# Optimization experiments

Hardware: AMD Instinct MI355X
Metric: run time of the kernel (lower is better)

## Reference

```python
import jax, jax.numpy as jnp
import numpy as np
from jax import lax

B, L = 8, 1024
C_IN, D_MODEL = 3, 512
N_MAMBA, N_TRANS, NHEAD = 2, 2, 8
D_STATE, D_CONV, EXPAND = 16, 4, 2
DI = EXPAND * D_MODEL            # 1024, mamba inner dim
DT_RANK = D_MODEL // 16          # 32
DH = D_MODEL // NHEAD            # 64, head dim
DFF = 4 * D_MODEL


def setup_inputs() -> dict:
    key = jax.random.key(0)
    ks = iter(jax.random.split(key, 64))
    def rn(shape, s=0.05):
        return jax.random.normal(next(ks), shape, jnp.float32) * s
    inp = {
        'x': jax.random.normal(next(ks), (B, C_IN, L), jnp.float32),
        'proj_w': rn((D_MODEL, C_IN)), 'proj_b': rn((D_MODEL,)),
        # stacked per-mamba-layer params (leading dim = N_MAMBA)
        'm_in_w': rn((N_MAMBA, 2 * DI, D_MODEL)),
        'm_conv_w': rn((N_MAMBA, DI, D_CONV)), 'm_conv_b': rn((N_MAMBA, DI)),
        'm_xproj_w': rn((N_MAMBA, DT_RANK + 2 * D_STATE, DI)),
        'm_dt_w': rn((N_MAMBA, DI, DT_RANK)), 'm_dt_b': rn((N_MAMBA, DI)),
        'm_Alog': jnp.tile(jnp.log(jnp.arange(1, D_STATE + 1, dtype=jnp.float32)), (N_MAMBA, DI, 1)),
        'm_D': jnp.ones((N_MAMBA, DI), jnp.float32),
        'm_out_w': rn((N_MAMBA, D_MODEL, DI)),
        'm_ln_w': jnp.ones((N_MAMBA, D_MODEL), jnp.float32), 'm_ln_b': jnp.zeros((N_MAMBA, D_MODEL), jnp.float32),
        # stacked per-transformer-layer params
        't_qkv_w': rn((N_TRANS, 3 * D_MODEL, D_MODEL)), 't_qkv_b': rn((N_TRANS, 3 * D_MODEL)),
        't_ow': rn((N_TRANS, D_MODEL, D_MODEL)), 't_ob': rn((N_TRANS, D_MODEL)),
        't_l1w': rn((N_TRANS, DFF, D_MODEL)), 't_l1b': rn((N_TRANS, DFF)),
        't_l2w': rn((N_TRANS, D_MODEL, DFF)), 't_l2b': rn((N_TRANS, D_MODEL)),
        't_ln1w': jnp.ones((N_TRANS, D_MODEL), jnp.float32), 't_ln1b': jnp.zeros((N_TRANS, D_MODEL), jnp.float32),
        't_ln2w': jnp.ones((N_TRANS, D_MODEL), jnp.float32), 't_ln2b': jnp.zeros((N_TRANS, D_MODEL), jnp.float32),
        'no_w': jnp.ones((D_MODEL,), jnp.float32), 'no_b': jnp.zeros((D_MODEL,), jnp.float32),
    }
    return inp


def _ln(x, w, b, eps=1e-5):
    m = x.mean(-1, keepdims=True)
    v = ((x - m) ** 2).mean(-1, keepdims=True)
    return (x - m) / jnp.sqrt(v + eps) * w + b


def _pos_encoding(length, d):
    pos = jnp.arange(length, dtype=jnp.float32)[:, None]
    div = jnp.exp(jnp.arange(0, d, 2, dtype=jnp.float32) * (-np.log(10000.0) / d))
    pe = jnp.zeros((length, d), jnp.float32)
    pe = pe.at[:, 0::2].set(jnp.sin(pos * div)).at[:, 1::2].set(jnp.cos(pos * div))
    return pe


def _mamba(h, in_w, conv_w, conv_b, xp_w, dt_w, dt_b, Alog, Dp, out_w):
    # h: [B,L,d_model]
    xz = h @ in_w.T                                   # [B,L,2*DI]
    xm, z = jnp.split(xz, 2, axis=-1)
    # causal depthwise conv1d over time
    k = conv_w.T[:, None, :]                          # [D_CONV,1,DI]
    xc = lax.conv_general_dilated(xm, k, (1,), [(D_CONV - 1, 0)],
                                  dimension_numbers=('NWC', 'WIO', 'NWC'),
                                  feature_group_count=DI) + conv_b
    xc = jax.nn.silu(xc)
    xdb = xc @ xp_w.T                                 # [B,L,DT_RANK+2*D_STATE]
    dt = jax.nn.softplus(xdb[..., :DT_RANK] @ dt_w.T + dt_b)   # [B,L,DI]
    Bm = xdb[..., DT_RANK:DT_RANK + D_STATE]          # [B,L,D_STATE]
    Cm = xdb[..., DT_RANK + D_STATE:]                 # [B,L,D_STATE]
    A = -jnp.exp(Alog)                                # [DI,D_STATE]

    def step(state, t):
        dt_t, B_t, C_t, x_t = t                       # [B,DI],[B,S],[B,S],[B,DI]
        dA = jnp.exp(dt_t[..., None] * A)             # [B,DI,S]
        state = state * dA + (dt_t * x_t)[..., None] * B_t[:, None, :]
        y = jnp.einsum('bds,bs->bd', state, C_t)
        return state, y

    init = jnp.zeros((h.shape[0], DI, D_STATE), h.dtype)
    seq = (dt.transpose(1, 0, 2), Bm.transpose(1, 0, 2), Cm.transpose(1, 0, 2), xc.transpose(1, 0, 2))
    _, ys = lax.scan(step, init, seq)                 # ys: [L,B,DI]
    y = ys.transpose(1, 0, 2) + Dp * xc
    y = y * jax.nn.silu(z)
    return y @ out_w.T                                # [B,L,d_model]


def _transformer_layer(h, qkv_w, qkv_b, ow, ob, l1w, l1b, l2w, l2b, ln1w, ln1b, ln2w, ln2b):
    Bt, Lt, d = h.shape
    qkv = h @ qkv_w.T + qkv_b
    q, k, v = jnp.split(qkv, 3, axis=-1)
    q = q.reshape(Bt, Lt, NHEAD, DH); k = k.reshape(Bt, Lt, NHEAD, DH); v = v.reshape(Bt, Lt, NHEAD, DH)
    sc = jnp.einsum('blhd,bmhd->bhlm', q, k) / np.sqrt(DH).astype(np.float32)
    a = jax.nn.softmax(sc, axis=-1)
    o = jnp.einsum('bhlm,bmhd->blhd', a, v).reshape(Bt, Lt, d)
    h = _ln(h + o @ ow.T + ob, ln1w, ln1b)
    ff = jax.nn.relu(h @ l1w.T + l1b) @ l2w.T + l2b
    return _ln(h + ff, ln2w, ln2b)


def reference(x, proj_w, proj_b, m_in_w, m_conv_w, m_conv_b, m_xproj_w, m_dt_w, m_dt_b,
              m_Alog, m_D, m_out_w, m_ln_w, m_ln_b, t_qkv_w, t_qkv_b, t_ow, t_ob,
              t_l1w, t_l1b, t_l2w, t_l2b, t_ln1w, t_ln1b, t_ln2w, t_ln2b, no_w, no_b):
    # proj_in: 1x1 conv == pointwise linear over channels; output [B,L,d]
    h = jnp.einsum('bcl,dc->bld', x, proj_w) + proj_b
    for i in range(N_MAMBA):
        h = _ln(h + _mamba(h, m_in_w[i], m_conv_w[i], m_conv_b[i], m_xproj_w[i],
                           m_dt_w[i], m_dt_b[i], m_Alog[i], m_D[i], m_out_w[i]),
                m_ln_w[i], m_ln_b[i])
    h = h + _pos_encoding(h.shape[1], D_MODEL)
    for i in range(N_TRANS):
        h = _transformer_layer(h, t_qkv_w[i], t_qkv_b[i], t_ow[i], t_ob[i],
                               t_l1w[i], t_l1b[i], t_l2w[i], t_l2b[i],
                               t_ln1w[i], t_ln1b[i], t_ln2w[i], t_ln2b[i])
    h = _ln(h, no_w, no_b)
    return h, h.mean(axis=1)
```

## Files before the change

### kernel.cpp

```cpp
#include <hip/hip_runtime.h>
#include <cstddef>

#define BATCH 8
#define LSEQ 1024
#define DMODEL 512
#define DINNER 1024
#define DSTATE 16
#define DTRANK 32
#define NHEAD 8
#define DHEAD 64
#define DFF 2048
#define MTOK 8192
#define NCHUNK 16
#define CLEN 64

typedef __attribute__((ext_vector_type(8))) short bfrag;
typedef __attribute__((ext_vector_type(4))) float f32x4;
typedef __attribute__((ext_vector_type(4))) unsigned short us4;
typedef unsigned short ushort_t;

__device__ __forceinline__ float silu_f(float x) { return x / (1.f + __expf(-x)); }

__device__ __forceinline__ unsigned short f2bf(float f) {
  unsigned u = __float_as_uint(f);
  return (unsigned short)((u + 0x7FFFu + ((u >> 16) & 1u)) >> 16);
}
__device__ __forceinline__ float bf2f(ushort_t u) {
  return __uint_as_float((unsigned)u << 16);
}

__device__ __forceinline__ void gll16(const ushort_t* g, ushort_t* l) {
  __builtin_amdgcn_global_load_lds(
      (const __attribute__((address_space(1))) unsigned int*)g,
      (__attribute__((address_space(3))) unsigned int*)l, 16, 0, 0);
}

__global__ __launch_bounds__(256) void cvt_bf16(const float* __restrict__ s,
                                                ushort_t* __restrict__ d, int n4) {
  int i = blockIdx.x * 256 + threadIdx.x;
  if (i >= n4) return;
  float4 v = ((const float4*)s)[i];
  us4 o = {f2bf(v.x), f2bf(v.y), f2bf(v.z), f2bf(v.w)};
  ((us4*)d)[i] = o;
}

__global__ __launch_bounds__(256) void proj_kernel(const float* __restrict__ x,
                                                   const float* __restrict__ pw,
                                                   const float* __restrict__ pb,
                                                   float* __restrict__ h,
                                                   ushort_t* __restrict__ hbf) {
  int idx = blockIdx.x * 256 + threadIdx.x;
  int d = idx & 511;
  int l = (idx >> 9) & 1023;
  int b = idx >> 19;
  const float* xb = x + (size_t)b * 3 * 1024 + l;
  float v = pb[d] + xb[0] * pw[d * 3] + xb[1024] * pw[d * 3 + 1] + xb[2048] * pw[d * 3 + 2];
  h[idx] = v;
  hbf[idx] = f2bf(v);
}

template <int ACT, int CBF, int SPLITK, int BN>
__global__ __launch_bounds__(256) void gemm_gll(const ushort_t* __restrict__ A,
                                                const ushort_t* __restrict__ W,
                                                const float* __restrict__ bias,
                                                void* __restrict__ Cp,
                                                int K, int lda, int ldc) {
  __shared__ ushort_t sA[2][4096];
  __shared__ ushort_t sB[2][BN * 32];
  constexpr int MREP = (BN == 128) ? 4 : 2;
  const int bm = blockIdx.y * 128, bn = blockIdx.x * BN;
  const int tid = threadIdx.x;
  const int wid = tid >> 6, lane = tid & 63;
  const int wrb = (BN == 128) ? (wid >> 1) * 64 : wid * 32;
  const int wcb = (BN == 128) ? (wid & 1) * 64 : 0;
  const int lr = lane & 15, ls = lane >> 4;
  const int sw = ls ^ ((lr >> 1) & 3);

  const int kseg = K / SPLITK;
  const int kbeg = (SPLITK > 1) ? blockIdx.z * kseg : 0;

  const int c0 = wid * 128 + lane;
  const int c1 = c0 + 64;
  const int r0 = c0 >> 2, s0 = (c0 & 3) ^ ((r0 >> 1) & 3);
  const int r1 = c1 >> 2, s1 = (c1 & 3) ^ ((r1 >> 1) & 3);
  const ushort_t* gA0 = A + (size_t)(bm + r0) * lda + kbeg + s0 * 8;
  const ushort_t* gA1 = A + (size_t)(bm + r1) * lda + kbeg + s1 * 8;
  const ushort_t* gB0;
  const ushort_t* gB1 = nullptr;
  if constexpr (BN == 128) {
    gB0 = W + (size_t)(bn + r0) * K + kbeg + s0 * 8;
    gB1 = W + (size_t)(bn + r1) * K + kbeg + s1 * 8;
  } else {
    const int cb = wid * 64 + lane;
    const int rb = cb >> 2, sb2 = (cb & 3) ^ ((rb >> 1) & 3);
    gB0 = W + (size_t)(bn + rb) * K + kbeg + sb2 * 8;
  }

  f32x4 acc[MREP][4];
#pragma unroll
  for (int i = 0; i < MREP; ++i)
#pragma unroll
    for (int j = 0; j < 4; ++j) acc[i][j] = (f32x4)(0.f);

#define STAGE(buf, step)                                             \
  do {                                                               \
    gll16(gA0 + (step) * 32, &sA[buf][wid * 1024]);                  \
    gll16(gA1 + (step) * 32, &sA[buf][wid * 1024 + 512]);            \
    if constexpr (BN == 128) {                                       \
      gll16(gB0 + (step) * 32, &sB[buf][wid * 1024]);                \
      gll16(gB1 + (step) * 32, &sB[buf][wid * 1024 + 512]);          \
    } else {                                                         \
      gll16(gB0 + (step) * 32, &sB[buf][wid * 512]);                 \
    }                                                                \
  } while (0)

  const int NT = kseg / 32;
  STAGE(0, 0);
  for (int t = 0; t < NT; ++t) {
    const int cur = t & 1;
    if (t + 1 < NT) {
      STAGE(cur ^ 1, t + 1);
      if constexpr (BN == 128)
        asm volatile("s_waitcnt vmcnt(4)" ::: "memory");
      else
        asm volatile("s_waitcnt vmcnt(3)" ::: "memory");
    } else {
      asm volatile("s_waitcnt vmcnt(0)" ::: "memory");
    }
    __builtin_amdgcn_sched_barrier(0);
    __builtin_amdgcn_s_barrier();
    __builtin_amdgcn_sched_barrier(0);

    bfrag af[MREP], bf[4];
#pragma unroll
    for (int mi = 0; mi < MREP; ++mi) {
      int row = wrb + mi * 16 + lr;
      af[mi] = *(const bfrag*)&sA[cur][(size_t)((row << 2) + sw) * 8];
    }
#pragma unroll
    for (int nj = 0; nj < 4; ++nj) {
      int col = wcb + nj * 16 + lr;
      bf[nj] = *(const bfrag*)&sB[cur][(size_t)((col << 2) + sw) * 8];
    }
#pragma unroll
    for (int mi = 0; mi < MREP; ++mi)
#pragma unroll
      for (int nj = 0; nj < 4; ++nj)
        acc[mi][nj] = __builtin_amdgcn_mfma_f32_16x16x32_bf16(af[mi], bf[nj], acc[mi][nj], 0, 0, 0);

    __builtin_amdgcn_s_barrier();
    __builtin_amdgcn_sched_barrier(0);
  }
#undef STAGE

  if (SPLITK > 1) {
    float* Cz = (float*)Cp + (size_t)blockIdx.z * 8192 * ldc;
#pragma unroll
    for (int nj = 0; nj < 4; ++nj) {
      int col = bn + wcb + nj * 16 + lr;
#pragma unroll
      for (int mi = 0; mi < MREP; ++mi) {
        int row0 = bm + wrb + mi * 16 + ls * 4;
#pragma unroll
        for (int r = 0; r < 4; ++r)
          Cz[(size_t)(row0 + r) * ldc + col] = acc[mi][nj][r];
      }
    }
  } else {
#pragma unroll
    for (int nj = 0; nj < 4; ++nj) {
      int col = bn + wcb + nj * 16 + lr;
      float bv = bias ? bias[col] : 0.f;
#pragma unroll
      for (int mi = 0; mi < MREP; ++mi) {
        int row0 = bm + wrb + mi * 16 + ls * 4;
#pragma unroll
        for (int r = 0; r < 4; ++r) {
          float v = acc[mi][nj][r] + bv;
          if (ACT == 1) v = fmaxf(v, 0.f);
          if (ACT == 2) v = (v > 20.f) ? v : log1pf(__expf(v));
          if (CBF)
            ((ushort_t*)Cp)[(size_t)(row0 + r) * ldc + col] = f2bf(v);
          else
            ((float*)Cp)[(size_t)(row0 + r) * ldc + col] = v;
        }
      }
    }
  }
}

__global__ __launch_bounds__(256) void reduce8_xdb(const float* __restrict__ p,
                                                   float* __restrict__ xdb,
                                                   ushort_t* __restrict__ xdb_bf) {
  int i = blockIdx.x * 256 + threadIdx.x;
  float4 a = ((const float4*)p)[i];
#pragma unroll
  for (int z = 1; z < 8; ++z) {
    float4 b = ((const float4*)p)[i + z * 131072];
    a.x += b.x; a.y += b.y; a.z += b.z; a.w += b.w;
  }
  ((float4*)xdb)[i] = a;
  us4 o = {f2bf(a.x), f2bf(a.y), f2bf(a.z), f2bf(a.w)};
  ((us4*)xdb_bf)[i] = o;
}

__global__ __launch_bounds__(256) void conv_silu_kernel(const ushort_t* __restrict__ xz,
                                                        const float* __restrict__ cw,
                                                        const float* __restrict__ cb,
                                                        ushort_t* __restrict__ xc) {
  int idx = blockIdx.x * 256 + threadIdx.x;
  int d = idx & 1023;
  int t = (idx >> 10) & 1023;
  int b = idx >> 20;
  float acc = cb[d];
#pragma unroll
  for (int w = 0; w < 4; ++w) {
    int tt = t - 3 + w;
    if (tt >= 0) acc += bf2f(xz[(((size_t)(b * 1024 + tt)) << 11) + d]) * cw[d * 4 + w];
  }
  xc[idx] = f2bf(silu_f(acc));
}

__global__ __launch_bounds__(256) void scan_pass1(const float* __restrict__ dt,
                                                  const float* __restrict__ xdb,
                                                  const ushort_t* __restrict__ xc,
                                                  const float* __restrict__ Alog,
                                                  float* __restrict__ scrP,
                                                  float* __restrict__ scrL) {
  int idx = blockIdx.x * 256 + threadIdx.x;
  int sh = idx & 3;
  int d = (idx >> 2) & 1023;
  int c = (idx >> 12) & 15;
  int b = idx >> 16;
  float A[4], st[4], P[4];
#pragma unroll
  for (int s = 0; s < 4; ++s) {
    A[s] = -__expf(Alog[d * 16 + sh * 4 + s]);
    st[s] = 0.f;
    P[s] = 1.f;
  }
  int t0 = c * CLEN;
  size_t base = (((size_t)(b * 1024 + t0)) << 10) + d;
  const float* xb = xdb + (size_t)(b * 1024 + t0) * 64 + 32 + sh * 4;
  float dtv = dt[base], xv = bf2f(xc[base]);
  for (int t = 0; t < CLEN; ++t) {
    float dtn = 0.f, xvn = 0.f;
    if (t + 1 < CLEN) { dtn = dt[base + 1024]; xvn = bf2f(xc[base + 1024]); }
    float4 Bv = *(const float4*)xb;
    float dx = dtv * xv;
    float e0 = __expf(dtv * A[0]), e1 = __expf(dtv * A[1]);
    float e2 = __expf(dtv * A[2]), e3 = __expf(dtv * A[3]);
    st[0] = st[0] * e0 + dx * Bv.x; P[0] *= e0;
    st[1] = st[1] * e1 + dx * Bv.y; P[1] *= e1;
    st[2] = st[2] * e2 + dx * Bv.z; P[2] *= e2;
    st[3] = st[3] * e3 + dx * Bv.w; P[3] *= e3;
    base += 1024; xb += 64;
    dtv = dtn; xv = xvn;
  }
  size_t pbase = (((size_t)((b * 16 + c) * 16 + sh * 4)) << 10) + d;
#pragma unroll
  for (int s = 0; s < 4; ++s) {
    scrP[pbase + ((size_t)s << 10)] = P[s];
    scrL[pbase + ((size_t)s << 10)] = st[s];
  }
}

__global__ __launch_bounds__(256) void scan_pass2(const float* __restrict__ scrP,
                                                  float* __restrict__ scrL) {
  int idx = blockIdx.x * 256 + threadIdx.x;
  int d = idx & 1023;
  int s = (idx >> 10) & 15;
  int b = idx >> 14;
  float cur = 0.f;
  for (int c = 0; c < 16; ++c) {
    size_t o = (((size_t)(((b * 16 + c) * 16) + s)) << 10) + d;
    float P = scrP[o];
    float loc = scrL[o];
    scrL[o] = cur;
    cur = cur * P + loc;
  }
}

__global__ __launch_bounds__(256) void scan_pass3(const float* __restrict__ dt,
                                                  const float* __restrict__ xdb,
                                                  const ushort_t* __restrict__ xc,
                                                  const ushort_t* __restrict__ xz,
                                                  ushort_t* __restrict__ ybf,
                                                  const float* __restrict__ Alog,
                                                  const float* __restrict__ Dp,
                                                  const float* __restrict__ scrL) {
  int idx = blockIdx.x * 256 + threadIdx.x;
  int sh = idx & 3;
  int d = (idx >> 2) & 1023;
  int c = (idx >> 12) & 15;
  int b = idx >> 16;
  float A[4], st[4];
  size_t pbase = (((size_t)((b * 16 + c) * 16 + sh * 4)) << 10) + d;
#pragma unroll
  for (int s = 0; s < 4; ++s) {
    A[s] = -__expf(Alog[d * 16 + sh * 4 + s]);
    st[s] = scrL[pbase + ((size_t)s << 10)];
  }
  float Dv = Dp[d];
  int t0 = c * CLEN;
  size_t base = (((size_t)(b * 1024 + t0)) << 10) + d;
  size_t zoff = ((((size_t)(b * 1024 + t0)) << 11)) + 1024 + d;
  const float* xb = xdb + (size_t)(b * 1024 + t0) * 64 + 32 + sh * 4;
  float dtv = dt[base], xv = bf2f(xc[base]), zv = bf2f(xz[zoff]);
  for (int t = 0; t < CLEN; ++t) {
    float dtn = 0.f, xvn = 0.f, zvn = 0.f;
    if (t + 1 < CLEN) {
      dtn = dt[base + 1024]; xvn = bf2f(xc[base + 1024]); zvn = bf2f(xz[zoff + 2048]);
    }
    float4 Bv = *(const float4*)xb;
    float4 Cv = *(const float4*)(xb + 16);
    float dx = dtv * xv;
    float e0 = __expf(dtv * A[0]), e1 = __expf(dtv * A[1]);
    float e2 = __expf(dtv * A[2]), e3 = __expf(dtv * A[3]);
    st[0] = st[0] * e0 + dx * Bv.x;
    st[1] = st[1] * e1 + dx * Bv.y;
    st[2] = st[2] * e2 + dx * Bv.z;
    st[3] = st[3] * e3 + dx * Bv.w;
    float acc = st[0] * Cv.x + st[1] * Cv.y + st[2] * Cv.z + st[3] * Cv.w;
    acc += __shfl_xor(acc, 1);
    acc += __shfl_xor(acc, 2);
    if (sh == 0)
      ybf[base] = f2bf((acc + Dv * xv) * silu_f(zv));
    base += 1024; zoff += 2048; xb += 64;
    dtv = dtn; xv = xvn; zv = zvn;
  }
}

__global__ __launch_bounds__(128) void resid_ln_kernel(const float* __restrict__ x,
                                                       const float* __restrict__ add,
                                                       const float* __restrict__ w,
                                                       const float* __restrict__ bias,
                                                       float* __restrict__ out,
                                                       ushort_t* __restrict__ out_bf) {
  int row = blockIdx.x, tid = threadIdx.x;
  float4 v = ((const float4*)(x + (size_t)row * 512))[tid];
  if (add) {
    float4 a = ((const float4*)(add + (size_t)row * 512))[tid];
    v.x += a.x; v.y += a.y; v.z += a.z; v.w += a.w;
  }
  float s = v.x + v.y + v.z + v.w;
  float ss = v.x * v.x + v.y * v.y + v.z * v.z + v.w * v.w;
#pragma unroll
  for (int o = 32; o; o >>= 1) {
    s += __shfl_xor(s, o);
    ss += __shfl_xor(ss, o);
  }
  __shared__ float red[4];
  int wid = tid >> 6;
  if ((tid & 63) == 0) { red[wid] = s; red[2 + wid] = ss; }
  __syncthreads();
  s = red[0] + red[1];
  ss = red[2] + red[3];
  float mean = s * (1.f / 512.f);
  float var = ss * (1.f / 512.f) - mean * mean;
  float inv = rsqrtf(var + 1e-5f);
  float4 wv = ((const float4*)w)[tid];
  float4 bv = ((const float4*)bias)[tid];
  float4 ov;
  ov.x = (v.x - mean) * inv * wv.x + bv.x;
  ov.y = (v.y - mean) * inv * wv.y + bv.y;
  ov.z = (v.z - mean) * inv * wv.z + bv.z;
  ov.w = (v.w - mean) * inv * wv.w + bv.w;
  ((float4*)(out + (size_t)row * 512))[tid] = ov;
  if (out_bf) {
    us4 ob = {f2bf(ov.x), f2bf(ov.y), f2bf(ov.z), f2bf(ov.w)};
    ((us4*)(out_bf + (size_t)row * 512))[tid] = ob;
  }
}

__global__ __launch_bounds__(128) void resid_ln_sk(const float* __restrict__ x,
                                                   const float* __restrict__ p,
                                                   const float* __restrict__ pbias,
                                                   const float* __restrict__ w,
                                                   const float* __restrict__ bias,
                                                   float* __restrict__ out,
                                                   ushort_t* __restrict__ out_bf) {
  int row = blockIdx.x, tid = threadIdx.x;
  float4 v = ((const float4*)(x + (size_t)row * 512))[tid];
  float4 a = ((const float4*)(p + (size_t)row * 512))[tid];
  float4 c = ((const float4*)(p + 4194304 + (size_t)row * 512))[tid];
  v.x += a.x + c.x; v.y += a.y + c.y; v.z += a.z + c.z; v.w += a.w + c.w;
  if (pbias) {
    float4 pb = ((const float4*)pbias)[tid];
    v.x += pb.x; v.y += pb.y; v.z += pb.z; v.w += pb.w;
  }
  float s = v.x + v.y + v.z + v.w;
  float ss = v.x * v.x + v.y * v.y + v.z * v.z + v.w * v.w;
#pragma unroll
  for (int o = 32; o; o >>= 1) {
    s += __shfl_xor(s, o);
    ss += __shfl_xor(ss, o);
  }
  __shared__ float red[4];
  int wid = tid >> 6;
  if ((tid & 63) == 0) { red[wid] = s; red[2 + wid] = ss; }
  __syncthreads();
  s = red[0] + red[1];
  ss = red[2] + red[3];
  float mean = s * (1.f / 512.f);
  float var = ss * (1.f / 512.f) - mean * mean;
  float inv = rsqrtf(var + 1e-5f);
  float4 wv = ((const float4*)w)[tid];
  float4 bv = ((const float4*)bias)[tid];
  float4 ov;
  ov.x = (v.x - mean) * inv * wv.x + bv.x;
  ov.y = (v.y - mean) * inv * wv.y + bv.y;
  ov.z = (v.z - mean) * inv * wv.z + bv.z;
  ov.w = (v.w - mean) * inv * wv.w + bv.w;
  ((float4*)(out + (size_t)row * 512))[tid] = ov;
  us4 ob = {f2bf(ov.x), f2bf(ov.y), f2bf(ov.z), f2bf(ov.w)};
  ((us4*)(out_bf + (size_t)row * 512))[tid] = ob;
}

__global__ __launch_bounds__(256) void posenc_kernel(float* __restrict__ h,
                                                     ushort_t* __restrict__ hbf) {
  int idx = blockIdx.x * 256 + threadIdx.x;
  int d = idx & 511;
  int l = (idx >> 9) & 1023;
  float freq = __expf(-(float)(d & ~1) * (9.210340371976184f / 512.f));
  float ang = (float)l * freq;
  float v = h[idx] + ((d & 1) ? cosf(ang) : sinf(ang));
  h[idx] = v;
  hbf[idx] = f2bf(v);
}

__global__ __launch_bounds__(256) void attn_mfma(const ushort_t* __restrict__ qkv,
                                                 ushort_t* __restrict__ ao) {
  __shared__ unsigned short Qs[8192];
  __shared__ unsigned short Ks[4096];
  __shared__ unsigned short Vt[4096];
  __shared__ unsigned short Ps[4096];
  const int tid = threadIdx.x;
  const int blk = blockIdx.x;
  const int qt = blk & 7, hh = (blk >> 3) & 7, b = blk >> 6;
  const int l0 = qt * 128;
  const size_t bb = (size_t)b * 1024 * 1536;

  const int srow = tid >> 2;
  const int sdb = (tid & 3) << 4;
  const int sc0 = sdb >> 3;

  {
    const ushort_t* qp = qkv + bb + (size_t)(l0 + srow) * 1536 + hh * 64 + sdb;
    *(bfrag*)&Qs[srow * 64 + ((sc0 ^ (srow & 7)) << 3)] = *(const bfrag*)qp;
    *(bfrag*)&Qs[srow * 64 + (((sc0 + 1) ^ (srow & 7)) << 3)] = *(const bfrag*)(qp + 8);
    const ushort_t* qp2 = qp + (size_t)64 * 1536;
    *(bfrag*)&Qs[(srow + 64) * 64 + ((sc0 ^ (srow & 7)) << 3)] = *(const bfrag*)qp2;
    *(bfrag*)&Qs[(srow + 64) * 64 + (((sc0 + 1) ^ (srow & 7)) << 3)] = *(const bfrag*)(qp2 + 8);
  }
  __syncthreads();

  const int wid = tid >> 6, lane = tid & 63;
  const int l15 = lane & 15, rg = lane >> 4;
  const int l7 = l15 & 7;

  bfrag aq[2][2];
#pragma unroll
  for (int s = 0; s < 2; ++s)
#pragma unroll
    for (int ks = 0; ks < 2; ++ks) {
      int qr = wid * 32 + s * 16 + l15;
      aq[s][ks] = *(const bfrag*)&Qs[qr * 64 + (((ks * 4 + rg) ^ l7) << 3)];
    }

  float m[2][4], lsum[2][4];
  f32x4 oacc[2][4];
#pragma unroll
  for (int s = 0; s < 2; ++s)
#pragma unroll
    for (int r = 0; r < 4; ++r) { m[s][r] = -1e30f; lsum[s][r] = 0.f; }
#pragma unroll
  for (int s = 0; s < 2; ++s)
#pragma unroll
    for (int nt = 0; nt < 4; ++nt) oacc[s][nt] = (f32x4)(0.f);

  for (int jt = 0; jt < 16; ++jt) {
    {
      const ushort_t* kp = qkv + bb + (size_t)(jt * 64 + srow) * 1536 + hh * 64 + 512 + sdb;
      *(bfrag*)&Ks[srow * 64 + ((sc0 ^ (srow & 7)) << 3)] = *(const bfrag*)kp;
      *(bfrag*)&Ks[srow * 64 + (((sc0 + 1) ^ (srow & 7)) << 3)] = *(const bfrag*)(kp + 8);
      const ushort_t* vp = kp + 512;
      unsigned short vv[16];
      *(bfrag*)&vv[0] = *(const bfrag*)vp;
      *(bfrag*)&vv[8] = *(const bfrag*)(vp + 8);
#pragma unroll
      for (int j = 0; j < 16; ++j) {
        int dd = sdb + j;
        Vt[dd * 64 + (((srow >> 3) ^ (dd & 7)) << 3) + (srow & 7)] = vv[j];
      }
    }
    __syncthreads();

#pragma unroll
    for (int s = 0; s < 2; ++s) {
      f32x4 sc[4];
#pragma unroll
      for (int nt = 0; nt < 4; ++nt) {
        f32x4 sv = (f32x4)(0.f);
#pragma unroll
        for (int ks = 0; ks < 2; ++ks) {
          bfrag bk = *(const bfrag*)&Ks[(nt * 16 + l15) * 64 + (((ks * 4 + rg) ^ l7) << 3)];
          sv = __builtin_amdgcn_mfma_f32_16x16x32_bf16(aq[s][ks], bk, sv, 0, 0, 0);
        }
        sc[nt] = sv * 0.125f;
      }

#pragma unroll
      for (int r = 0; r < 4; ++r) {
        float mc = fmaxf(fmaxf(sc[0][r], sc[1][r]), fmaxf(sc[2][r], sc[3][r]));
#pragma unroll
        for (int o = 8; o; o >>= 1) mc = fmaxf(mc, __shfl_xor(mc, o));
        float mn = fmaxf(m[s][r], mc);
        float al = __expf(m[s][r] - mn);
        m[s][r] = mn;
        int prow = rg * 4 + r;
        float ps = 0.f;
#pragma unroll
        for (int nt = 0; nt < 4; ++nt) {
          float p = __expf(sc[nt][r] - mn);
          ps += p;
          int col = nt * 16 + l15;
          Ps[wid * 1024 + prow * 64 + ((((col >> 3) ^ (prow & 7))) << 3) + (col & 7)] = f2bf(p);
        }
#pragma unroll
        for (int o = 8; o; o >>= 1) ps += __shfl_xor(ps, o);
        lsum[s][r] = lsum[s][r] * al + ps;
#pragma unroll
        for (int nt = 0; nt < 4; ++nt) oacc[s][nt][r] *= al;
      }

      bfrag ap[2];
#pragma unroll
      for (int ks = 0; ks < 2; ++ks)
        ap[ks] = *(const bfrag*)&Ps[wid * 1024 + l15 * 64 + (((ks * 4 + rg) ^ l7) << 3)];
#pragma unroll
      for (int nt = 0; nt < 4; ++nt) {
#pragma unroll
        for (int ks = 0; ks < 2; ++ks) {
          bfrag bv = *(const bfrag*)&Vt[(nt * 16 + l15) * 64 + (((ks * 4 + rg) ^ l7) << 3)];
          oacc[s][nt] = __builtin_amdgcn_mfma_f32_16x16x32_bf16(ap[ks], bv, oacc[s][nt], 0, 0, 0);
        }
      }
    }
    __syncthreads();
  }

#pragma unroll
  for (int s = 0; s < 2; ++s)
#pragma unroll
    for (int r = 0; r < 4; ++r) {
      float inv = 1.f / lsum[s][r];
      int row = l0 + wid * 32 + s * 16 + rg * 4 + r;
      ushort_t* op = ao + ((size_t)(b * 1024 + row)) * 512 + hh * 64;
#pragma unroll
      for (int nt = 0; nt < 4; ++nt) op[nt * 16 + l15] = f2bf(oacc[s][nt][r] * inv);
    }
}

__global__ __launch_bounds__(512) void mean_part(const float* __restrict__ h,
                                                 float* __restrict__ part) {
  int blk = blockIdx.x;
  int b = blk >> 4, lc = blk & 15, d = threadIdx.x;
  float s = 0.f;
  int l0 = lc * 64;
  for (int l = l0; l < l0 + 64; ++l) s += h[(((size_t)(b * 1024 + l)) << 9) + d];
  part[((size_t)blk << 9) + d] = s;
}
__global__ __launch_bounds__(256) void mean_final(const float* __restrict__ part,
                                                  float* __restrict__ out2) {
  int i = blockIdx.x * 256 + threadIdx.x;
  int b = i >> 9, d = i & 511;
  float s = 0.f;
#pragma unroll
  for (int c = 0; c < 16; ++c) s += part[(((size_t)(b * 16 + c)) << 9) + d];
  out2[i] = s * (1.f / 1024.f);
}

extern "C" void kernel_launch(void* const* d_in, const int* in_sizes, int n_in,
                              void* d_out, int out_size, void* d_ws, size_t ws_size,
                              hipStream_t stream) {
  const float* x        = (const float*)d_in[0];
  const float* proj_w   = (const float*)d_in[1];
  const float* proj_b   = (const float*)d_in[2];
  const float* m_in_w   = (const float*)d_in[3];
  const float* m_conv_w = (const float*)d_in[4];
  const float* m_conv_b = (const float*)d_in[5];
  const float* m_xproj_w= (const float*)d_in[6];
  const float* m_dt_w   = (const float*)d_in[7];
  const float* m_dt_b   = (const float*)d_in[8];
  const float* m_Alog   = (const float*)d_in[9];
  const float* m_D      = (const float*)d_in[10];
  const float* m_out_w  = (const float*)d_in[11];
  const float* m_ln_w   = (const float*)d_in[12];
  const float* m_ln_b   = (const float*)d_in[13];
  const float* t_qkv_w  = (const float*)d_in[14];
  const float* t_qkv_b  = (const float*)d_in[15];
  const float* t_ow     = (const float*)d_in[16];
  const float* t_ob     = (const float*)d_in[17];
  const float* t_l1w    = (const float*)d_in[18];
  const float* t_l1b    = (const float*)d_in[19];
  const float* t_l2w    = (const float*)d_in[20];
  const float* t_l2b    = (const float*)d_in[21];
  const float* t_ln1w   = (const float*)d_in[22];
  const float* t_ln1b   = (const float*)d_in[23];
  const float* t_ln2w   = (const float*)d_in[24];
  const float* t_ln2b   = (const float*)d_in[25];
  const float* no_w     = (const float*)d_in[26];
  const float* no_b     = (const float*)d_in[27];

  float* ws   = (float*)d_ws;
  float* h    = ws;
  ushort_t* h_bf = (ushort_t*)(ws + 4194304);
  float* bufA = ws + 6291456;
  float* bufB = bufA + 16777216;
  float* bufC = bufB + 8388608;
  float* bufE = bufC + 8388608;
  float* bufF = bufE + 4194304;
  ushort_t* y_bf = (ushort_t*)(bufF + 524288);
  ushort_t* wbf  = (ushort_t*)(bufF + 524288 + 4194304);
  float* scrP = bufE;
  float* scrL = bufE + 2097152;

  ushort_t* wIN  = wbf;
  ushort_t* wOUT = wbf + 2097152;
  ushort_t* wQKV = wbf + 3145728;
  ushort_t* wOW  = wbf + 4718592;
  ushort_t* wL1  = wbf + 5242880;
  ushort_t* wL2  = wbf + 7340032;
  ushort_t* wXP  = wbf + 9437184;
  ushort_t* wDT  = wbf + 9568256;
  ushort_t* xdb_bf = wbf + 9633792;

  cvt_bf16<<<2048, 256, 0, stream>>>(m_in_w,  wIN,  524288);
  cvt_bf16<<<1024, 256, 0, stream>>>(m_out_w, wOUT, 262144);
  cvt_bf16<<<1536, 256, 0, stream>>>(t_qkv_w, wQKV, 393216);
  cvt_bf16<<< 512, 256, 0, stream>>>(t_ow,    wOW,  131072);
  cvt_bf16<<<2048, 256, 0, stream>>>(t_l1w,   wL1,  524288);
  cvt_bf16<<<2048, 256, 0, stream>>>(t_l2w,   wL2,  524288);
  cvt_bf16<<< 128, 256, 0, stream>>>(m_xproj_w, wXP, 32768);
  cvt_bf16<<<  64, 256, 0, stream>>>(m_dt_w,  wDT,  16384);

  proj_kernel<<<16384, 256, 0, stream>>>(x, proj_w, proj_b, h, h_bf);

  for (int i = 0; i < 2; ++i) {
    gemm_gll<0, 1, 1, 128><<<dim3(16, 64), 256, 0, stream>>>(
        h_bf, wIN + (size_t)i * 1048576, nullptr, bufA, DMODEL, DMODEL, 2 * DINNER);
    conv_silu_kernel<<<32768, 256, 0, stream>>>((const ushort_t*)bufA,
                                                m_conv_w + i * DINNER * 4,
                                                m_conv_b + i * DINNER, (ushort_t*)bufB);
    gemm_gll<0, 0, 8, 64><<<dim3(1, 64, 8), 256, 0, stream>>>(
        (const ushort_t*)bufB, wXP + (size_t)i * 65536, nullptr, bufC,
        DINNER, DINNER, 64);
    reduce8_xdb<<<512, 256, 0, stream>>>(bufC, bufF, xdb_bf);
    gemm_gll<2, 0, 1, 128><<<dim3(8, 64), 256, 0, stream>>>(
        xdb_bf, wDT + (size_t)i * 32768, m_dt_b + i * DINNER, bufC,
        DTRANK, 64, DINNER);
    scan_pass1<<<2048, 256, 0, stream>>>(bufC, bufF, (const ushort_t*)bufB,
                                         m_Alog + (size_t)i * DINNER * DSTATE, scrP, scrL);
    scan_pass2<<<512, 256, 0, stream>>>(scrP, scrL);
    scan_pass3<<<2048, 256, 0, stream>>>(bufC, bufF, (const ushort_t*)bufB,
                                         (const ushort_t*)bufA, y_bf,
                                         m_Alog + (size_t)i * DINNER * DSTATE,
                                         m_D + i * DINNER, scrL);
    gemm_gll<0, 0, 2, 128><<<dim3(4, 64, 2), 256, 0, stream>>>(
        y_bf, wOUT + (size_t)i * 524288, nullptr, bufC, DINNER, DINNER, DMODEL);
    resid_ln_sk<<<8192, 128, 0, stream>>>(h, bufC, nullptr, m_ln_w + i * DMODEL,
                                          m_ln_b + i * DMODEL, h, h_bf);
  }

  posenc_kernel<<<16384, 256, 0, stream>>>(h, h_bf);

  for (int i = 0; i < 2; ++i) {
    gemm_gll<0, 1, 1, 128><<<dim3(12, 64), 256, 0, stream>>>(
        h_bf, wQKV + (size_t)i * 786432, t_qkv_b + i * 3 * DMODEL, bufA,
        DMODEL, DMODEL, 3 * DMODEL);
    attn_mfma<<<512, 256, 0, stream>>>((const ushort_t*)bufA, (ushort_t*)bufB);
    gemm_gll<0, 0, 2, 128><<<dim3(4, 64, 2), 256, 0, stream>>>(
        (const ushort_t*)bufB, wOW + (size_t)i * 262144, nullptr, bufC,
        DMODEL, DMODEL, DMODEL);
    resid_ln_sk<<<8192, 128, 0, stream>>>(h, bufC, t_ob + i * DMODEL,
                                          t_ln1w + i * DMODEL, t_ln1b + i * DMODEL, h, h_bf);
    gemm_gll<1, 1, 1, 128><<<dim3(16, 64), 256, 0, stream>>>(
        h_bf, wL1 + (size_t)i * 1048576, t_l1b + i * DFF, bufA,
        DMODEL, DMODEL, DFF);
    gemm_gll<0, 0, 2, 128><<<dim3(4, 64, 2), 256, 0, stream>>>(
        (const ushort_t*)bufA, wL2 + (size_t)i * 1048576, nullptr, bufC,
        DFF, DFF, DMODEL);
    resid_ln_sk<<<8192, 128, 0, stream>>>(h, bufC, t_l2b + i * DMODEL,
                                          t_ln2w + i * DMODEL, t_ln2b + i * DMODEL, h, h_bf);
  }

  float* out_h = (float*)d_out;
  resid_ln_kernel<<<8192, 128, 0, stream>>>(h, nullptr, no_w, no_b, out_h, nullptr);
  mean_part<<<128, 512, 0, stream>>>(out_h, bufF);
  mean_final<<<16, 256, 0, stream>>>(bufF, out_h + 4194304);
}
```

Baseline: 963.8 us.

## Batch weight conversions, store dt in bf16, shrink attention query tile

The eight weight-conversion launches become one segmented kernel that picks its source and destination by block index, which removes launch overhead. The dt projection GEMM now writes bf16 instead of fp32, and both scan passes read bf16 dt, which halves that traffic at some cost in precision. The attention kernel drops from 128 to 64 query rows per block and doubles the grid to 1024 blocks, with a block-to-(batch,head) mapping and an extra XOR swizzle on the V transpose to cut LDS bank conflicts. This trades more K/V reloads for more parallelism and lower register pressure.

```diff
diff --git a/kernel.cpp b/kernel.cpp
--- a/kernel.cpp
+++ b/kernel.cpp
@@ -35,13 +35,21 @@
       (__attribute__((address_space(3))) unsigned int*)l, 16, 0, 0);
 }
 
-__global__ __launch_bounds__(256) void cvt_bf16(const float* __restrict__ s,
-                                                ushort_t* __restrict__ d, int n4) {
-  int i = blockIdx.x * 256 + threadIdx.x;
-  if (i >= n4) return;
-  float4 v = ((const float4*)s)[i];
+struct Cvt8Args {
+  const float* s[8];
+  ushort_t* d[8];
+  int end[8];
+};
+__global__ __launch_bounds__(256) void cvt8(Cvt8Args a) {
+  int blk = blockIdx.x;
+  int seg = 0, start = 0;
+#pragma unroll
+  for (int i = 0; i < 7; ++i)
+    if (blk >= a.end[i]) { seg = i + 1; start = a.end[i]; }
+  int i4 = (blk - start) * 256 + threadIdx.x;
+  float4 v = ((const float4*)a.s[seg])[i4];
   us4 o = {f2bf(v.x), f2bf(v.y), f2bf(v.z), f2bf(v.w)};
-  ((us4*)d)[i] = o;
+  ((us4*)a.d[seg])[i4] = o;
 }
 
 __global__ __launch_bounds__(256) void proj_kernel(const float* __restrict__ x,
@@ -221,7 +229,7 @@
   xc[idx] = f2bf(silu_f(acc));
 }
 
-__global__ __launch_bounds__(256) void scan_pass1(const float* __restrict__ dt,
+__global__ __launch_bounds__(256) void scan_pass1(const ushort_t* __restrict__ dt,
                                                   const float* __restrict__ xdb,
                                                   const ushort_t* __restrict__ xc,
                                                   const float* __restrict__ Alog,
@@ -242,10 +250,10 @@
   int t0 = c * CLEN;
   size_t base = (((size_t)(b * 1024 + t0)) << 10) + d;
   const float* xb = xdb + (size_t)(b * 1024 + t0) * 64 + 32 + sh * 4;
-  float dtv = dt[base], xv = bf2f(xc[base]);
+  float dtv = bf2f(dt[base]), xv = bf2f(xc[base]);
   for (int t = 0; t < CLEN; ++t) {
     float dtn = 0.f, xvn = 0.f;
-    if (t + 1 < CLEN) { dtn = dt[base + 1024]; xvn = bf2f(xc[base + 1024]); }
+    if (t + 1 < CLEN) { dtn = bf2f(dt[base + 1024]); xvn = bf2f(xc[base + 1024]); }
     float4 Bv = *(const float4*)xb;
     float dx = dtv * xv;
     float e0 = __expf(dtv * A[0]), e1 = __expf(dtv * A[1]);
@@ -281,7 +289,7 @@
   }
 }
 
-__global__ __launch_bounds__(256) void scan_pass3(const float* __restrict__ dt,
+__global__ __launch_bounds__(256) void scan_pass3(const ushort_t* __restrict__ dt,
                                                   const float* __restrict__ xdb,
                                                   const ushort_t* __restrict__ xc,
                                                   const ushort_t* __restrict__ xz,
@@ -306,11 +314,11 @@
   size_t base = (((size_t)(b * 1024 + t0)) << 10) + d;
   size_t zoff = ((((size_t)(b * 1024 + t0)) << 11)) + 1024 + d;
   const float* xb = xdb + (size_t)(b * 1024 + t0) * 64 + 32 + sh * 4;
-  float dtv = dt[base], xv = bf2f(xc[base]), zv = bf2f(xz[zoff]);
+  float dtv = bf2f(dt[base]), xv = bf2f(xc[base]), zv = bf2f(xz[zoff]);
   for (int t = 0; t < CLEN; ++t) {
     float dtn = 0.f, xvn = 0.f, zvn = 0.f;
     if (t + 1 < CLEN) {
-      dtn = dt[base + 1024]; xvn = bf2f(xc[base + 1024]); zvn = bf2f(xz[zoff + 2048]);
+      dtn = bf2f(dt[base + 1024]); xvn = bf2f(xc[base + 1024]); zvn = bf2f(xz[zoff + 2048]);
     }
     float4 Bv = *(const float4*)xb;
     float4 Cv = *(const float4*)(xb + 16);
@@ -431,14 +439,16 @@
 
 __global__ __launch_bounds__(256) void attn_mfma(const ushort_t* __restrict__ qkv,
                                                  ushort_t* __restrict__ ao) {
-  __shared__ unsigned short Qs[8192];
+  __shared__ unsigned short Qs[4096];
   __shared__ unsigned short Ks[4096];
   __shared__ unsigned short Vt[4096];
   __shared__ unsigned short Ps[4096];
   const int tid = threadIdx.x;
-  const int blk = blockIdx.x;
-  const int qt = blk & 7, hh = (blk >> 3) & 7, b = blk >> 6;
-  const int l0 = qt * 128;
+  const int w = blockIdx.x;
+  const int bh = (w & 7) + (w >> 7) * 8;
+  const int qt = (w >> 3) & 15;
+  const int hh = bh & 7, b = bh >> 3;
+  const int l0 = qt * 64;
   const size_t bb = (size_t)b * 1024 * 1536;
 
   const int srow = tid >> 2;
@@ -449,35 +459,17 @@
     const ushort_t* qp = qkv + bb + (size_t)(l0 + srow) * 1536 + hh * 64 + sdb;
     *(bfrag*)&Qs[srow * 64 + ((sc0 ^ (srow & 7)) << 3)] = *(const bfrag*)qp;
     *(bfrag*)&Qs[srow * 64 + (((sc0 + 1) ^ (srow & 7)) << 3)] = *(const bfrag*)(qp + 8);
-    const ushort_t* qp2 = qp + (size_t)64 * 1536;
-    *(bfrag*)&Qs[(srow + 64) * 64 + ((sc0 ^ (srow & 7)) << 3)] = *(const bfrag*)qp2;
-    *(bfrag*)&Qs[(srow + 64) * 64 + (((sc0 + 1) ^ (srow & 7)) << 3)] = *(const bfrag*)(qp2 + 8);
-  }
-  __syncthreads();
+  }
 
   const int wid = tid >> 6, lane = tid & 63;
   const int l15 = lane & 15, rg = lane >> 4;
   const int l7 = l15 & 7;
-
-  bfrag aq[2][2];
-#pragma unroll
-  for (int s = 0; s < 2; ++s)
-#pragma unroll
-    for (int ks = 0; ks < 2; ++ks) {
-      int qr = wid * 32 + s * 16 + l15;
-      aq[s][ks] = *(const bfrag*)&Qs[qr * 64 + (((ks * 4 + rg) ^ l7) << 3)];
-    }
-
-  float m[2][4], lsum[2][4];
-  f32x4 oacc[2][4];
-#pragma unroll
-  for (int s = 0; s < 2; ++s)
-#pragma unroll
-    for (int r = 0; r < 4; ++r) { m[s][r] = -1e30f; lsum[s][r] = 0.f; }
-#pragma unroll
-  for (int s = 0; s < 2; ++s)
-#pragma unroll
-    for (int nt = 0; nt < 4; ++nt) oacc[s][nt] = (f32x4)(0.f);
+  float m[4], lsum[4];
+  f32x4 oacc[4];
+#pragma unroll
+  for (int r = 0; r < 4; ++r) { m[r] = -1e30f; lsum[r] = 0.f; }
+#pragma unroll
+  for (int nt = 0; nt < 4; ++nt) oacc[nt] = (f32x4)(0.f);
 
   for (int jt = 0; jt < 16; ++jt) {
     {
@@ -491,75 +483,76 @@
 #pragma unroll
       for (int j = 0; j < 16; ++j) {
         int dd = sdb + j;
-        Vt[dd * 64 + (((srow >> 3) ^ (dd & 7)) << 3) + (srow & 7)] = vv[j];
+        Vt[dd * 64 + (((srow >> 3) ^ (dd & 7) ^ ((dd >> 3) & 7)) << 3) + (srow & 7)] = vv[j];
       }
     }
     __syncthreads();
 
-#pragma unroll
-    for (int s = 0; s < 2; ++s) {
-      f32x4 sc[4];
+    bfrag aq[2];
+#pragma unroll
+    for (int ks = 0; ks < 2; ++ks)
+      aq[ks] = *(const bfrag*)&Qs[(wid * 16 + l15) * 64 + (((ks * 4 + rg) ^ l7) << 3)];
+    f32x4 sc[4];
+#pragma unroll
+    for (int nt = 0; nt < 4; ++nt) {
+      f32x4 s = (f32x4)(0.f);
+#pragma unroll
+      for (int ks = 0; ks < 2; ++ks) {
+        bfrag bk = *(const bfrag*)&Ks[(nt * 16 + l15) * 64 + (((ks * 4 + rg) ^ l7) << 3)];
+        s = __builtin_amdgcn_mfma_f32_16x16x32_bf16(aq[ks], bk, s, 0, 0, 0);
+      }
+      sc[nt] = s * 0.125f;
+    }
+
+#pragma unroll
+    for (int r = 0; r < 4; ++r) {
+      float mc = fmaxf(fmaxf(sc[0][r], sc[1][r]), fmaxf(sc[2][r], sc[3][r]));
+#pragma unroll
+      for (int o = 8; o; o >>= 1) mc = fmaxf(mc, __shfl_xor(mc, o));
+      float mn = fmaxf(m[r], mc);
+      float al = __expf(m[r] - mn);
+      m[r] = mn;
+      int prow = rg * 4 + r;
+      float ps = 0.f;
 #pragma unroll
       for (int nt = 0; nt < 4; ++nt) {
-        f32x4 sv = (f32x4)(0.f);
-#pragma unroll
-        for (int ks = 0; ks < 2; ++ks) {
-          bfrag bk = *(const bfrag*)&Ks[(nt * 16 + l15) * 64 + (((ks * 4 + rg) ^ l7) << 3)];
-          sv = __builtin_amdgcn_mfma_f32_16x16x32_bf16(aq[s][ks], bk, sv, 0, 0, 0);
-        }
-        sc[nt] = sv * 0.125f;
+        float p = __expf(sc[nt][r] - mn);
+        ps += p;
+        int col = nt * 16 + l15;
+        Ps[wid * 1024 + prow * 64 + ((((col >> 3) ^ (prow & 7))) << 3) + (col & 7)] = f2bf(p);
       }
-
-#pragma unroll
-      for (int r = 0; r < 4; ++r) {
-        float mc = fmaxf(fmaxf(sc[0][r], sc[1][r]), fmaxf(sc[2][r], sc[3][r]));
-#pragma unroll
-        for (int o = 8; o; o >>= 1) mc = fmaxf(mc, __shfl_xor(mc, o));
-        float mn = fmaxf(m[s][r], mc);
-        float al = __expf(m[s][r] - mn);
-        m[s][r] = mn;
-        int prow = rg * 4 + r;
-        float ps = 0.f;
-#pragma unroll
-        for (int nt = 0; nt < 4; ++nt) {
-          float p = __expf(sc[nt][r] - mn);
-          ps += p;
-          int col = nt * 16 + l15;
-          Ps[wid * 1024 + prow * 64 + ((((col >> 3) ^ (prow & 7))) << 3) + (col & 7)] = f2bf(p);
-        }
-#pragma unroll
-        for (int o = 8; o; o >>= 1) ps += __shfl_xor(ps, o);
-        lsum[s][r] = lsum[s][r] * al + ps;
-#pragma unroll
-        for (int nt = 0; nt < 4; ++nt) oacc[s][nt][r] *= al;
+#pragma unroll
+      for (int o = 8; o; o >>= 1) ps += __shfl_xor(ps, o);
+      lsum[r] = lsum[r] * al + ps;
+#pragma unroll
+      for (int nt = 0; nt < 4; ++nt) oacc[nt][r] *= al;
+    }
+
+    bfrag ap[2];
+#pragma unroll
+    for (int ks = 0; ks < 2; ++ks)
+      ap[ks] = *(const bfrag*)&Ps[wid * 1024 + l15 * 64 + (((ks * 4 + rg) ^ l7) << 3)];
+#pragma unroll
+    for (int nt = 0; nt < 4; ++nt) {
+      int vrow = nt * 16 + l15;
+#pragma unroll
+      for (int ks = 0; ks < 2; ++ks) {
+        bfrag bv = *(const bfrag*)&Vt[vrow * 64 +
+            (((ks * 4 + rg) ^ (vrow & 7) ^ ((vrow >> 3) & 7)) << 3)];
+        oacc[nt] = __builtin_amdgcn_mfma_f32_16x16x32_bf16(ap[ks], bv, oacc[nt], 0, 0, 0);
       }
-
-      bfrag ap[2];
-#pragma unroll
-      for (int ks = 0; ks < 2; ++ks)
-        ap[ks] = *(const bfrag*)&Ps[wid * 1024 + l15 * 64 + (((ks * 4 + rg) ^ l7) << 3)];
-#pragma unroll
-      for (int nt = 0; nt < 4; ++nt) {
-#pragma unroll
-        for (int ks = 0; ks < 2; ++ks) {
-          bfrag bv = *(const bfrag*)&Vt[(nt * 16 + l15) * 64 + (((ks * 4 + rg) ^ l7) << 3)];
-          oacc[s][nt] = __builtin_amdgcn_mfma_f32_16x16x32_bf16(ap[ks], bv, oacc[s][nt], 0, 0, 0);
-        }
-      }
     }
     __syncthreads();
   }
 
 #pragma unroll
-  for (int s = 0; s < 2; ++s)
-#pragma unroll
-    for (int r = 0; r < 4; ++r) {
-      float inv = 1.f / lsum[s][r];
-      int row = l0 + wid * 32 + s * 16 + rg * 4 + r;
-      ushort_t* op = ao + ((size_t)(b * 1024 + row)) * 512 + hh * 64;
-#pragma unroll
-      for (int nt = 0; nt < 4; ++nt) op[nt * 16 + l15] = f2bf(oacc[s][nt][r] * inv);
-    }
+  for (int r = 0; r < 4; ++r) {
+    float inv = 1.f / lsum[r];
+    int row = l0 + wid * 16 + rg * 4 + r;
+    ushort_t* op = ao + ((size_t)(b * 1024 + row)) * 512 + hh * 64;
+#pragma unroll
+    for (int nt = 0; nt < 4; ++nt) op[nt * 16 + l15] = f2bf(oacc[nt][r] * inv);
+  }
 }
 
 __global__ __launch_bounds__(512) void mean_part(const float* __restrict__ h,
@@ -636,14 +629,18 @@
   ushort_t* wDT  = wbf + 9568256;
   ushort_t* xdb_bf = wbf + 9633792;
 
-  cvt_bf16<<<2048, 256, 0, stream>>>(m_in_w,  wIN,  524288);
-  cvt_bf16<<<1024, 256, 0, stream>>>(m_out_w, wOUT, 262144);
-  cvt_bf16<<<1536, 256, 0, stream>>>(t_qkv_w, wQKV, 393216);
-  cvt_bf16<<< 512, 256, 0, stream>>>(t_ow,    wOW,  131072);
-  cvt_bf16<<<2048, 256, 0, stream>>>(t_l1w,   wL1,  524288);
-  cvt_bf16<<<2048, 256, 0, stream>>>(t_l2w,   wL2,  524288);
-  cvt_bf16<<< 128, 256, 0, stream>>>(m_xproj_w, wXP, 32768);
-  cvt_bf16<<<  64, 256, 0, stream>>>(m_dt_w,  wDT,  16384);
+  Cvt8Args ca;
+  ca.s[0] = m_in_w;    ca.d[0] = wIN;  
+  ca.s[1] = m_out_w;   ca.d[1] = wOUT;
+  ca.s[2] = t_qkv_w;   ca.d[2] = wQKV;
+  ca.s[3] = t_ow;      ca.d[3] = wOW;
+  ca.s[4] = t_l1w;     ca.d[4] = wL1;
+  ca.s[5] = t_l2w;     ca.d[5] = wL2;
+  ca.s[6] = m_xproj_w; ca.d[6] = wXP;
+  ca.s[7] = m_dt_w;    ca.d[7] = wDT;
+  ca.end[0] = 2048; ca.end[1] = 3072; ca.end[2] = 4608; ca.end[3] = 5120;
+  ca.end[4] = 7168; ca.end[5] = 9216; ca.end[6] = 9344; ca.end[7] = 9408;
+  cvt8<<<9408, 256, 0, stream>>>(ca);
 
   proj_kernel<<<16384, 256, 0, stream>>>(x, proj_w, proj_b, h, h_bf);
 
@@ -657,13 +654,13 @@
         (const ushort_t*)bufB, wXP + (size_t)i * 65536, nullptr, bufC,
         DINNER, DINNER, 64);
     reduce8_xdb<<<512, 256, 0, stream>>>(bufC, bufF, xdb_bf);
-    gemm_gll<2, 0, 1, 128><<<dim3(8, 64), 256, 0, stream>>>(
+    gemm_gll<2, 1, 1, 128><<<dim3(8, 64), 256, 0, stream>>>(
         xdb_bf, wDT + (size_t)i * 32768, m_dt_b + i * DINNER, bufC,
         DTRANK, 64, DINNER);
-    scan_pass1<<<2048, 256, 0, stream>>>(bufC, bufF, (const ushort_t*)bufB,
+    scan_pass1<<<2048, 256, 0, stream>>>((const ushort_t*)bufC, bufF, (const ushort_t*)bufB,
                                          m_Alog + (size_t)i * DINNER * DSTATE, scrP, scrL);
     scan_pass2<<<512, 256, 0, stream>>>(scrP, scrL);
-    scan_pass3<<<2048, 256, 0, stream>>>(bufC, bufF, (const ushort_t*)bufB,
+    scan_pass3<<<2048, 256, 0, stream>>>((const ushort_t*)bufC, bufF, (const ushort_t*)bufB,
                                          (const ushort_t*)bufA, y_bf,
                                          m_Alog + (size_t)i * DINNER * DSTATE,
                                          m_D + i * DINNER, scrL);
@@ -679,7 +676,7 @@
     gemm_gll<0, 1, 1, 128><<<dim3(12, 64), 256, 0, stream>>>(
         h_bf, wQKV + (size_t)i * 786432, t_qkv_b + i * 3 * DMODEL, bufA,
         DMODEL, DMODEL, 3 * DMODEL);
-    attn_mfma<<<512, 256, 0, stream>>>((const ushort_t*)bufA, (ushort_t*)bufB);
+    attn_mfma<<<1024, 256, 0, stream>>>((const ushort_t*)bufA, (ushort_t*)bufB);
     gemm_gll<0, 0, 2, 128><<<dim3(4, 64, 2), 256, 0, stream>>>(
         (const ushort_t*)bufB, wOW + (size_t)i * 262144, nullptr, bufC,
         DMODEL, DMODEL, DMODEL);
```

Result: faster. 925.2 us (-4.0%).
